# Performance work log

Hardware: AMD Instinct MI355X
Metric: run time of the kernel (lower is better)

## Reference

```python
import jax, jax.numpy as jnp
import numpy as np

D = 32  # embedding_dimension (TGN default memory_dimension == embedding_dimension)


def time_encode(t, w, b):
    # TGN TimeEncode: cos(t * w + b); t: [E] -> [E, D]
    return jnp.cos(t[:, None] * w[None, :] + b[None, :])


def setup_inputs() -> dict:
    key = jax.random.key(0)
    ks = jax.random.split(key, 24)
    N, B, E, F, NE = 1_000_000, 262_144, 1_048_576, 64, 500_000
    inp = {}
    # per-node-type memory tables (Mailbox memory)
    inp["mem_user"] = jax.random.normal(ks[0], (N, D), jnp.float32)
    inp["mem_item"] = jax.random.normal(ks[1], (N, D), jnp.float32)
    # active event node ids per type (memory lookup indices)
    inp["node_ids_user"] = jax.random.randint(ks[2], (B,), 0, N, jnp.int32)
    inp["node_ids_item"] = jax.random.randint(ks[3], (B,), 0, N, jnp.int32)
    # heterogeneous edge lists: user->item and item->user (indices into the B active nodes)
    inp["edge_src_ui"] = jax.random.randint(ks[4], (E,), 0, B, jnp.int32)
    inp["edge_dst_ui"] = jax.random.randint(ks[5], (E,), 0, B, jnp.int32)
    inp["edge_src_iu"] = jax.random.randint(ks[6], (E,), 0, B, jnp.int32)
    inp["edge_dst_iu"] = jax.random.randint(ks[7], (E,), 0, B, jnp.int32)
    inp["edge_idx_ui"] = jax.random.randint(ks[8], (E,), 0, NE, jnp.int32)
    inp["edge_idx_iu"] = jax.random.randint(ks[9], (E,), 0, NE, jnp.int32)
    inp["edge_rel_times_ui"] = jax.random.uniform(ks[10], (E,), jnp.float32) * 1000.0
    inp["edge_rel_times_iu"] = jax.random.uniform(ks[11], (E,), jnp.float32) * 1000.0
    inp["edge_feature"] = jax.random.normal(ks[12], (NE, F), jnp.float32)
    # per-node-type Linear(D, D, bias=False) == self.lin[node_type]
    s = 1.0 / np.sqrt(D)
    inp["W_user"] = jax.random.normal(ks[13], (D, D), jnp.float32) * s
    inp["W_item"] = jax.random.normal(ks[14], (D, D), jnp.float32) * s
    # per-edge-type Linear(F, D) == self.edge_feature_linear[edge_type]
    se = 1.0 / np.sqrt(F)
    inp["We_ui"] = jax.random.normal(ks[15], (F, D), jnp.float32) * se
    inp["be_ui"] = jnp.zeros((D,), jnp.float32)
    inp["We_iu"] = jax.random.normal(ks[16], (F, D), jnp.float32) * se
    inp["be_iu"] = jnp.zeros((D,), jnp.float32)
    # TimeEncode params (standard TGN init: 1/10^linspace)
    inp["time_w"] = jnp.asarray(1.0 / (10.0 ** np.linspace(0, 9, D)), jnp.float32)
    inp["time_b"] = jnp.zeros((D,), jnp.float32)
    # decoder(2*D -> 64 -> 16 -> 1), drop=0
    inp["dec_W1"] = jax.random.normal(ks[17], (2 * D, 64), jnp.float32) * (1.0 / np.sqrt(2 * D))
    inp["dec_b1"] = jnp.zeros((64,), jnp.float32)
    inp["dec_W2"] = jax.random.normal(ks[18], (64, 16), jnp.float32) * 0.125
    inp["dec_b2"] = jnp.zeros((16,), jnp.float32)
    inp["dec_W3"] = jax.random.normal(ks[19], (16, 1), jnp.float32) * 0.25
    inp["dec_b3"] = jnp.zeros((1,), jnp.float32)
    return inp


def reference(mem_user, mem_item, edge_feature, edge_rel_times_ui, edge_rel_times_iu,
              W_user, W_item, We_ui, be_ui, We_iu, be_iu, time_w, time_b,
              dec_W1, dec_b1, dec_W2, dec_b2, dec_W3, dec_b3,
              node_ids_user, node_ids_item, edge_src_ui, edge_dst_ui,
              edge_src_iu, edge_dst_iu, edge_idx_ui, edge_idx_iu):
    B = node_ids_user.shape[0]
    # memory lookup + per-node-type linear (self.lin[node_type], bias=False)
    h_user = mem_user[node_ids_user] @ W_user   # [B, D]
    h_item = mem_item[node_ids_item] @ W_item   # [B, D]
    # heterogeneous message passing: src memory + edge-feature linear + time encoding,
    # scattered (segment_sum) onto destination nodes per edge type
    msg_ui = (h_user[edge_src_ui]
              + edge_feature[edge_idx_ui] @ We_ui + be_ui
              + time_encode(edge_rel_times_ui, time_w, time_b))  # [E, D]
    agg_item = jax.ops.segment_sum(msg_ui, edge_dst_ui, num_segments=B)
    msg_iu = (h_item[edge_src_iu]
              + edge_feature[edge_idx_iu] @ We_iu + be_iu
              + time_encode(edge_rel_times_iu, time_w, time_b))  # [E, D]
    agg_user = jax.ops.segment_sum(msg_iu, edge_dst_iu, num_segments=B)
    hu = jax.nn.relu(h_user + agg_user)
    hi = jax.nn.relu(h_item + agg_item)
    # decoder `distance` on concatenated pair embeddings (2*D -> 64 -> 16 -> 1), drop=0
    z = jnp.concatenate([hu, hi], axis=-1)      # [B, 2D]
    x = jax.nn.relu(z @ dec_W1 + dec_b1)
    x = jax.nn.relu(x @ dec_W2 + dec_b2)
    return x @ dec_W3 + dec_b3                   # [B, 1]
```

## Files before the change

kernel.cpp:

```cpp
#include <hip/hip_runtime.h>

#define DEV __device__ __forceinline__

typedef __attribute__((ext_vector_type(8))) short short8;
typedef __attribute__((ext_vector_type(16))) float float16;
typedef __attribute__((ext_vector_type(4))) float f32x4;
typedef __attribute__((ext_vector_type(2))) unsigned int u32x2;
typedef __attribute__((ext_vector_type(4))) unsigned int u32x4;

DEV unsigned short f2bf(float x) {
    unsigned u = __float_as_uint(x);
    unsigned r = (u + 0x7FFFu + ((u >> 16) & 1u)) >> 16;
    return (unsigned short)r;
}
DEV unsigned pack_bf2(float a, float b) {
    return (unsigned)f2bf(a) | ((unsigned)f2bf(b) << 16);
}
DEV float bf2f(unsigned short v) {
    return __uint_as_float(((unsigned)v) << 16);
}
DEV float fastcos(float x) {
    float r = x * 0.15915494309189535f;
    r = r - floorf(r);
    return __builtin_amdgcn_cosf(r);
}

__global__ void prep_kernel(const float* __restrict__ W_user, const float* __restrict__ W_item,
                            const float* __restrict__ We_ui, const float* __restrict__ be_ui,
                            const float* __restrict__ We_iu, const float* __restrict__ be_iu,
                            const float* __restrict__ dW1, const float* __restrict__ dW2,
                            float* __restrict__ Wt_user, float* __restrict__ Wt_item,
                            unsigned short* __restrict__ Wb, float* __restrict__ bc,
                            float* __restrict__ W1t, float* __restrict__ W2t) {
    int t = threadIdx.x;
    for (int i = t; i < 1024; i += 256) {
        int k = i / 32, d = i % 32;
        Wt_user[d * 32 + k] = W_user[i];
        Wt_item[d * 32 + k] = W_item[i];
    }
    for (int i = t; i < 4096; i += 256) {
        int kt   = i >> 10;
        int rem  = i & 1023;
        int n2   = rem >> 9;
        int rem2 = rem & 511;
        int l    = rem2 >> 3;
        int ii   = rem2 & 7;
        int k = kt * 16 + (l >> 5) * 8 + ii;
        int n = (l & 31);
        float v = n2 ? We_iu[k * 32 + n] : We_ui[k * 32 + n];
        Wb[i] = f2bf(v);
    }
    for (int i = t; i < 64; i += 256)
        bc[i] = (i < 32) ? be_ui[i] : be_iu[i - 32];
    for (int i = t; i < 4096; i += 256) {
        int j = i / 64, k = i % 64;
        W1t[i] = dW1[k * 64 + j];
    }
    for (int i = t; i < 1024; i += 256) {
        int c = i / 64, j = i % 64;
        W2t[i] = dW2[j * 16 + c];
    }
}

__global__ __launch_bounds__(256) void node_linear_kernel(
        const float* __restrict__ mem, const int* __restrict__ ids,
        const float* __restrict__ Wt, float* __restrict__ h,
        unsigned short* __restrict__ h16, int B) {
    int r = blockIdx.x * 256 + threadIdx.x;
    if (r >= B) return;
    int id = ids[r];
    const f32x4* m4 = (const f32x4*)(mem + (size_t)id * 32);
    float m[32];
#pragma unroll
    for (int q = 0; q < 8; ++q) {
        f32x4 v = __builtin_nontemporal_load(m4 + q);
        m[4 * q + 0] = v[0]; m[4 * q + 1] = v[1]; m[4 * q + 2] = v[2]; m[4 * q + 3] = v[3];
    }
    float* hr = h + (size_t)r * 32;
    unsigned short* hr16 = h16 + (size_t)r * 32;
    for (int db = 0; db < 8; ++db) {
        float acc[4];
#pragma unroll
        for (int u = 0; u < 4; ++u) {
            const float* wr = Wt + (size_t)(db * 4 + u) * 32;
            float a = 0.f;
#pragma unroll
            for (int k = 0; k < 32; ++k) a = fmaf(m[k], wr[k], a);
            acc[u] = a;
        }
        f32x4 o; o[0] = acc[0]; o[1] = acc[1]; o[2] = acc[2]; o[3] = acc[3];
        __builtin_nontemporal_store(o, (f32x4*)(hr + db * 4));
        u32x2 p; p[0] = pack_bf2(acc[0], acc[1]); p[1] = pack_bf2(acc[2], acc[3]);
        *(u32x2*)(hr16 + db * 4) = p;
    }
}

__global__ __launch_bounds__(256) void proj_mfma_kernel(
        const float* __restrict__ feat, const unsigned short* __restrict__ Wb,
        const float* __restrict__ bc, unsigned short* __restrict__ proj, int NE) {
    __shared__ unsigned short lds[128 * 72];
    const int lane = threadIdx.x & 63;
    const int wave = threadIdx.x >> 6;
    const int col  = lane & 31;
    const int half = lane >> 5;

    short8 bfrag[8];
    const short8* wb8 = (const short8*)Wb;
#pragma unroll
    for (int f = 0; f < 8; ++f) bfrag[f] = wb8[f * 64 + lane];

    int r = blockIdx.x * 128 + wave * 32 + col;
    if (r >= NE) r = NE - 1;
    const float* fr = feat + (size_t)r * 64 + half * 8;
    short8 afrag[4];
#pragma unroll
    for (int t = 0; t < 4; ++t) {
        f32x4 a = __builtin_nontemporal_load((const f32x4*)(fr + t * 16));
        f32x4 b = __builtin_nontemporal_load((const f32x4*)(fr + t * 16 + 4));
        short8 s;
        s[0] = (short)f2bf(a[0]); s[1] = (short)f2bf(a[1]);
        s[2] = (short)f2bf(a[2]); s[3] = (short)f2bf(a[3]);
        s[4] = (short)f2bf(b[0]); s[5] = (short)f2bf(b[1]);
        s[6] = (short)f2bf(b[2]); s[7] = (short)f2bf(b[3]);
        afrag[t] = s;
    }

    float16 acc0, acc1;
    float b0 = bc[col], b1 = bc[32 + col];
#pragma unroll
    for (int i = 0; i < 16; ++i) { acc0[i] = b0; acc1[i] = b1; }
#pragma unroll
    for (int t = 0; t < 4; ++t) {
        acc0 = __builtin_amdgcn_mfma_f32_32x32x16_bf16(afrag[t], bfrag[t * 2 + 0], acc0, 0, 0, 0);
        acc1 = __builtin_amdgcn_mfma_f32_32x32x16_bf16(afrag[t], bfrag[t * 2 + 1], acc1, 0, 0, 0);
    }

#pragma unroll
    for (int reg = 0; reg < 16; ++reg) {
        int rl = wave * 32 + (reg & 3) + 8 * (reg >> 2) + 4 * half;
        lds[rl * 72 + col]      = f2bf(acc0[reg]);
        lds[rl * 72 + 32 + col] = f2bf(acc1[reg]);
    }
    __syncthreads();

    int trow = threadIdx.x >> 1, thalf = threadIdx.x & 1;
    int grow = blockIdx.x * 128 + trow;
    if (grow < NE) {
        const u32x4* lsrc = (const u32x4*)(lds + trow * 72 + thalf * 32);
        u32x4* gdst = (u32x4*)(proj + (size_t)grow * 64 + thalf * 32);
#pragma unroll
        for (int s = 0; s < 4; ++s) gdst[s] = lsrc[s];
    }
}

__global__ __launch_bounds__(256) void link_kernel(
        const int* __restrict__ src_ui, const int* __restrict__ dst_ui,
        const int* __restrict__ eidx_ui, const float* __restrict__ rt_ui,
        const int* __restrict__ src_iu, const int* __restrict__ dst_iu,
        const int* __restrict__ eidx_iu, const float* __restrict__ rt_iu,
        int* __restrict__ head, int4* __restrict__ edata, int E, int B) {
    int ge = blockIdx.x * 256 + threadIdx.x;
    if (ge >= 2 * E) return;
    int s, ix, d; float tv;
    if (ge < E) {
        s  = __builtin_nontemporal_load(src_ui + ge);
        ix = __builtin_nontemporal_load(eidx_ui + ge);
        tv = __builtin_nontemporal_load(rt_ui + ge);
        d  = __builtin_nontemporal_load(dst_ui + ge);
    } else {
        int e = ge - E;
        s  = __builtin_nontemporal_load(src_iu + e);
        ix = __builtin_nontemporal_load(eidx_iu + e);
        tv = __builtin_nontemporal_load(rt_iu + e);
        d  = __builtin_nontemporal_load(dst_iu + e) + B;
    }
    int nxt = atomicExch(head + d, ge);
    edata[ge] = make_int4(s, ix, __float_as_int(tv), nxt);
}

__global__ __launch_bounds__(256) void agg_kernel(
        const int4* __restrict__ edata, const int* __restrict__ head,
        const unsigned short* __restrict__ h16_user, const unsigned short* __restrict__ h16_item,
        const unsigned short* __restrict__ proj,
        float* __restrict__ agg_user, float* __restrict__ agg_item,
        const float* __restrict__ tw, const float* __restrict__ tb, int B) {
    int g = threadIdx.x >> 5, d = threadIdx.x & 31;
    int n = blockIdx.x * 8 + g;
    if (n >= 2 * B) return;
    int type = (n >= B);
    const unsigned short* h = type ? h16_item : h16_user;
    const unsigned short* pr = proj + (type ? 32 : 0) + d;
    float twd = tw[d], tbd = tb[d];
    float acc = 0.f;
    int e = head[n];
    while (e >= 0) {
        int4 cur = edata[e];
        float pv = bf2f(pr[(size_t)cur.y * 64]);
        float c  = fastcos(fmaf(__int_as_float(cur.z), twd, tbd));
        acc += bf2f(h[(size_t)cur.x * 32 + d]) + pv + c;
        e = cur.w;
    }
    if (type) agg_user[(size_t)(n - B) * 32 + d] = acc;
    else      agg_item[(size_t)n * 32 + d] = acc;
}

__global__ __launch_bounds__(256) void decoder_kernel(
        const float* __restrict__ h_user, const float* __restrict__ h_item,
        const float* __restrict__ agg_user, const float* __restrict__ agg_item,
        const float* __restrict__ W1t, const float* __restrict__ b1,
        const float* __restrict__ W2t, const float* __restrict__ b2,
        const float* __restrict__ W3, const float* __restrict__ b3,
        float* __restrict__ out, int B) {
    int i = blockIdx.x * 256 + threadIdx.x;
    if (i >= B) return;
    float z[64];
    {
        const f32x4* a4 = (const f32x4*)(h_user + (size_t)i * 32);
        const f32x4* b4 = (const f32x4*)(agg_user + (size_t)i * 32);
#pragma unroll
        for (int q = 0; q < 8; ++q) {
            f32x4 a = __builtin_nontemporal_load(a4 + q);
            f32x4 b = b4[q];
            z[4 * q + 0] = fmaxf(a[0] + b[0], 0.f);
            z[4 * q + 1] = fmaxf(a[1] + b[1], 0.f);
            z[4 * q + 2] = fmaxf(a[2] + b[2], 0.f);
            z[4 * q + 3] = fmaxf(a[3] + b[3], 0.f);
        }
    }
    {
        const f32x4* a4 = (const f32x4*)(h_item + (size_t)i * 32);
        const f32x4* b4 = (const f32x4*)(agg_item + (size_t)i * 32);
#pragma unroll
        for (int q = 0; q < 8; ++q) {
            f32x4 a = __builtin_nontemporal_load(a4 + q);
            f32x4 b = b4[q];
            z[32 + 4 * q + 0] = fmaxf(a[0] + b[0], 0.f);
            z[32 + 4 * q + 1] = fmaxf(a[1] + b[1], 0.f);
            z[32 + 4 * q + 2] = fmaxf(a[2] + b[2], 0.f);
            z[32 + 4 * q + 3] = fmaxf(a[3] + b[3], 0.f);
        }
    }
    float x2[16];
#pragma unroll
    for (int c = 0; c < 16; ++c) x2[c] = b2[c];
    for (int jb = 0; jb < 8; ++jb) {
        float a[8];
#pragma unroll
        for (int u = 0; u < 8; ++u) {
            int j = jb * 8 + u;
            const float* wr = W1t + (size_t)j * 64;
            float acc = b1[j];
#pragma unroll
            for (int k = 0; k < 64; ++k) acc = fmaf(z[k], wr[k], acc);
            a[u] = fmaxf(acc, 0.f);
        }
#pragma unroll
        for (int c = 0; c < 16; ++c) {
            const float* w2r = W2t + (size_t)c * 64 + jb * 8;
            float acc = x2[c];
#pragma unroll
            for (int u = 0; u < 8; ++u) acc = fmaf(a[u], w2r[u], acc);
            x2[c] = acc;
        }
    }
    float o = b3[0];
#pragma unroll
    for (int c = 0; c < 16; ++c) o = fmaf(fmaxf(x2[c], 0.f), W3[c], o);
    out[i] = o;
}

extern "C" void kernel_launch(void* const* d_in, const int* in_sizes, int n_in,
                              void* d_out, int out_size, void* d_ws, size_t ws_size,
                              hipStream_t stream) {
    const float* mem_user = (const float*)d_in[0];
    const float* mem_item = (const float*)d_in[1];
    const int*   ids_user = (const int*)d_in[2];
    const int*   ids_item = (const int*)d_in[3];
    const int*   src_ui   = (const int*)d_in[4];
    const int*   dst_ui   = (const int*)d_in[5];
    const int*   src_iu   = (const int*)d_in[6];
    const int*   dst_iu   = (const int*)d_in[7];
    const int*   eidx_ui  = (const int*)d_in[8];
    const int*   eidx_iu  = (const int*)d_in[9];
    const float* rt_ui    = (const float*)d_in[10];
    const float* rt_iu    = (const float*)d_in[11];
    const float* feat     = (const float*)d_in[12];
    const float* W_user   = (const float*)d_in[13];
    const float* W_item   = (const float*)d_in[14];
    const float* We_ui    = (const float*)d_in[15];
    const float* be_ui    = (const float*)d_in[16];
    const float* We_iu    = (const float*)d_in[17];
    const float* be_iu    = (const float*)d_in[18];
    const float* tw       = (const float*)d_in[19];
    const float* tb       = (const float*)d_in[20];
    const float* dW1      = (const float*)d_in[21];
    const float* db1      = (const float*)d_in[22];
    const float* dW2      = (const float*)d_in[23];
    const float* db2      = (const float*)d_in[24];
    const float* dW3      = (const float*)d_in[25];
    const float* db3      = (const float*)d_in[26];

    const int B  = in_sizes[2];
    const int E  = in_sizes[4];
    const int NE = in_sizes[12] / 64;
    const int NB2 = 2 * B;

    float* w = (float*)d_ws;
    const size_t hsz = (size_t)B * 32;
    float* h_user   = w;
    float* h_item   = h_user + hsz;
    float* agg_user = h_item + hsz;
    float* agg_item = agg_user + hsz;
    float* Wt_user  = agg_item + hsz;
    float* Wt_item  = Wt_user + 1024;
    unsigned short* Wb = (unsigned short*)(Wt_item + 1024);
    float* bc       = (float*)(Wb + 4096);
    float* W1t      = bc + 64;
    float* W2t      = W1t + 4096;
    unsigned short* proj = (unsigned short*)(W2t + 1024);
    int* head = (int*)(proj + (size_t)NE * 64);
    int4* edata = (int4*)(head + NB2);
    unsigned short* h16_user = (unsigned short*)(edata + (size_t)2 * E);
    unsigned short* h16_item = h16_user + hsz;

    prep_kernel<<<1, 256, 0, stream>>>(W_user, W_item, We_ui, be_ui, We_iu, be_iu, dW1, dW2,
                                       Wt_user, Wt_item, Wb, bc, W1t, W2t);
    (void)hipMemsetAsync(head, 0xFF, (size_t)NB2 * sizeof(int), stream);

    proj_mfma_kernel<<<(NE + 127) / 128, 256, 0, stream>>>(feat, Wb, bc, proj, NE);
    node_linear_kernel<<<(B + 255) / 256, 256, 0, stream>>>(mem_user, ids_user, Wt_user,
                                                            h_user, h16_user, B);
    node_linear_kernel<<<(B + 255) / 256, 256, 0, stream>>>(mem_item, ids_item, Wt_item,
                                                            h_item, h16_item, B);

    int e2blocks = (2 * E + 255) / 256;
    link_kernel<<<e2blocks, 256, 0, stream>>>(src_ui, dst_ui, eidx_ui, rt_ui,
                                              src_iu, dst_iu, eidx_iu, rt_iu,
                                              head, edata, E, B);
    agg_kernel<<<(NB2 + 7) / 8, 256, 0, stream>>>(edata, head, h16_user, h16_item, proj,
                                                  agg_user, agg_item, tw, tb, B);
    decoder_kernel<<<(B + 255) / 256, 256, 0, stream>>>(h_user, h_item, agg_user, agg_item,
                                                        W1t, db1, W2t, db2, dW3, db3,
                                                        (float*)d_out, B);
}
```

Baseline: 875.1 us.

## Split per-node edge linked lists into four chains for parallel traversal

The link kernel now spreads each destination node's edges over four separate list heads, chosen by the low bits of the edge id. The aggregation kernel then walks all four chains together, issuing up to four independent edata loads per iteration. This shortens each dependent pointer-chasing chain and raises memory-level parallelism, at the cost of a four-times-larger head array and memset, plus extra branching per iteration. Separately, nontemporal loads and stores in the node-linear and decoder kernels become ordinary accesses, so the h buffers can stay in cache for the decoder.

```diff
diff --git a/kernel.cpp b/kernel.cpp
--- a/kernel.cpp
+++ b/kernel.cpp
@@ -73,7 +73,7 @@
     float m[32];
 #pragma unroll
     for (int q = 0; q < 8; ++q) {
-        f32x4 v = __builtin_nontemporal_load(m4 + q);
+        f32x4 v = m4[q];
         m[4 * q + 0] = v[0]; m[4 * q + 1] = v[1]; m[4 * q + 2] = v[2]; m[4 * q + 3] = v[3];
     }
     float* hr = h + (size_t)r * 32;
@@ -89,7 +89,7 @@
             acc[u] = a;
         }
         f32x4 o; o[0] = acc[0]; o[1] = acc[1]; o[2] = acc[2]; o[3] = acc[3];
-        __builtin_nontemporal_store(o, (f32x4*)(hr + db * 4));
+        *(f32x4*)(hr + db * 4) = o;
         u32x2 p; p[0] = pack_bf2(acc[0], acc[1]); p[1] = pack_bf2(acc[2], acc[3]);
         *(u32x2*)(hr16 + db * 4) = p;
     }
@@ -174,12 +174,12 @@
         tv = __builtin_nontemporal_load(rt_iu + e);
         d  = __builtin_nontemporal_load(dst_iu + e) + B;
     }
-    int nxt = atomicExch(head + d, ge);
+    int nxt = atomicExch(head + (d << 2) + (ge & 3), ge);
     edata[ge] = make_int4(s, ix, __float_as_int(tv), nxt);
 }
 
 __global__ __launch_bounds__(256) void agg_kernel(
-        const int4* __restrict__ edata, const int* __restrict__ head,
+        const int4* __restrict__ edata, const int4* __restrict__ head4,
         const unsigned short* __restrict__ h16_user, const unsigned short* __restrict__ h16_item,
         const unsigned short* __restrict__ proj,
         float* __restrict__ agg_user, float* __restrict__ agg_item,
@@ -192,13 +192,34 @@
     const unsigned short* pr = proj + (type ? 32 : 0) + d;
     float twd = tw[d], tbd = tb[d];
     float acc = 0.f;
-    int e = head[n];
-    while (e >= 0) {
-        int4 cur = edata[e];
-        float pv = bf2f(pr[(size_t)cur.y * 64]);
-        float c  = fastcos(fmaf(__int_as_float(cur.z), twd, tbd));
-        acc += bf2f(h[(size_t)cur.x * 32 + d]) + pv + c;
-        e = cur.w;
+    int4 hd = head4[n];
+    int e0 = hd.x, e1 = hd.y, e2 = hd.z, e3 = hd.w;
+    while ((e0 & e1 & e2 & e3) >= 0) {
+        int4 c0, c1, c2, c3;
+        if (e0 >= 0) c0 = edata[e0];
+        if (e1 >= 0) c1 = edata[e1];
+        if (e2 >= 0) c2 = edata[e2];
+        if (e3 >= 0) c3 = edata[e3];
+        if (e0 >= 0) {
+            acc += bf2f(h[(size_t)c0.x * 32 + d]) + bf2f(pr[(size_t)c0.y * 64])
+                 + fastcos(fmaf(__int_as_float(c0.z), twd, tbd));
+            e0 = c0.w;
+        }
+        if (e1 >= 0) {
+            acc += bf2f(h[(size_t)c1.x * 32 + d]) + bf2f(pr[(size_t)c1.y * 64])
+                 + fastcos(fmaf(__int_as_float(c1.z), twd, tbd));
+            e1 = c1.w;
+        }
+        if (e2 >= 0) {
+            acc += bf2f(h[(size_t)c2.x * 32 + d]) + bf2f(pr[(size_t)c2.y * 64])
+                 + fastcos(fmaf(__int_as_float(c2.z), twd, tbd));
+            e2 = c2.w;
+        }
+        if (e3 >= 0) {
+            acc += bf2f(h[(size_t)c3.x * 32 + d]) + bf2f(pr[(size_t)c3.y * 64])
+                 + fastcos(fmaf(__int_as_float(c3.z), twd, tbd));
+            e3 = c3.w;
+        }
     }
     if (type) agg_user[(size_t)(n - B) * 32 + d] = acc;
     else      agg_item[(size_t)n * 32 + d] = acc;
@@ -219,8 +240,7 @@
         const f32x4* b4 = (const f32x4*)(agg_user + (size_t)i * 32);
 #pragma unroll
         for (int q = 0; q < 8; ++q) {
-            f32x4 a = __builtin_nontemporal_load(a4 + q);
-            f32x4 b = b4[q];
+            f32x4 a = a4[q], b = b4[q];
             z[4 * q + 0] = fmaxf(a[0] + b[0], 0.f);
             z[4 * q + 1] = fmaxf(a[1] + b[1], 0.f);
             z[4 * q + 2] = fmaxf(a[2] + b[2], 0.f);
@@ -232,8 +252,7 @@
         const f32x4* b4 = (const f32x4*)(agg_item + (size_t)i * 32);
 #pragma unroll
         for (int q = 0; q < 8; ++q) {
-            f32x4 a = __builtin_nontemporal_load(a4 + q);
-            f32x4 b = b4[q];
+            f32x4 a = a4[q], b = b4[q];
             z[32 + 4 * q + 0] = fmaxf(a[0] + b[0], 0.f);
             z[32 + 4 * q + 1] = fmaxf(a[1] + b[1], 0.f);
             z[32 + 4 * q + 2] = fmaxf(a[2] + b[2], 0.f);
@@ -319,13 +338,13 @@
     float* W2t      = W1t + 4096;
     unsigned short* proj = (unsigned short*)(W2t + 1024);
     int* head = (int*)(proj + (size_t)NE * 64);
-    int4* edata = (int4*)(head + NB2);
+    int4* edata = (int4*)(head + (size_t)NB2 * 4);
     unsigned short* h16_user = (unsigned short*)(edata + (size_t)2 * E);
     unsigned short* h16_item = h16_user + hsz;
 
     prep_kernel<<<1, 256, 0, stream>>>(W_user, W_item, We_ui, be_ui, We_iu, be_iu, dW1, dW2,
                                        Wt_user, Wt_item, Wb, bc, W1t, W2t);
-    (void)hipMemsetAsync(head, 0xFF, (size_t)NB2 * sizeof(int), stream);
+    (void)hipMemsetAsync(head, 0xFF, (size_t)NB2 * 4 * sizeof(int), stream);
 
     proj_mfma_kernel<<<(NE + 127) / 128, 256, 0, stream>>>(feat, Wb, bc, proj, NE);
     node_linear_kernel<<<(B + 255) / 256, 256, 0, stream>>>(mem_user, ids_user, Wt_user,
@@ -337,7 +356,8 @@
     link_kernel<<<e2blocks, 256, 0, stream>>>(src_ui, dst_ui, eidx_ui, rt_ui,
                                               src_iu, dst_iu, eidx_iu, rt_iu,
                                               head, edata, E, B);
-    agg_kernel<<<(NB2 + 7) / 8, 256, 0, stream>>>(edata, head, h16_user, h16_item, proj,
+    agg_kernel<<<(NB2 + 7) / 8, 256, 0, stream>>>(edata, (const int4*)head,
+                                                  h16_user, h16_item, proj,
                                                   agg_user, agg_item, tw, tb, B);
     decoder_kernel<<<(B + 255) / 256, 256, 0, stream>>>(h_user, h_item, agg_user, agg_item,
                                                         W1t, db1, W2t, db2, dW3, db3,
```

Result: no change. 862.5 us (-1.4%).

## Replace linked-list edge chains with counting-sort CSR for aggregation

Applied to the files above, without the earlier changes.

Replaces the atomicExch linked-list construction with a histogram, a three-pass prefix scan, and an atomic scatter that builds a per-destination permutation (CSR-like). The aggregation kernel then iterates over contiguous index ranges, unrolled by four, so independent gathers can be in flight at once instead of chasing a serial pointer chain. Several nontemporal loads and stores are also changed to regular accesses. It adds extra kernel launches, a second pass over the destination arrays, and one more indirection per edge (perm then edata).

```diff
diff --git a/kernel.cpp b/kernel.cpp
--- a/kernel.cpp
+++ b/kernel.cpp
@@ -73,7 +73,7 @@
     float m[32];
 #pragma unroll
     for (int q = 0; q < 8; ++q) {
-        f32x4 v = __builtin_nontemporal_load(m4 + q);
+        f32x4 v = m4[q];
         m[4 * q + 0] = v[0]; m[4 * q + 1] = v[1]; m[4 * q + 2] = v[2]; m[4 * q + 3] = v[3];
     }
     float* hr = h + (size_t)r * 32;
@@ -89,7 +89,7 @@
             acc[u] = a;
         }
         f32x4 o; o[0] = acc[0]; o[1] = acc[1]; o[2] = acc[2]; o[3] = acc[3];
-        __builtin_nontemporal_store(o, (f32x4*)(hr + db * 4));
+        *(f32x4*)(hr + db * 4) = o;
         u32x2 p; p[0] = pack_bf2(acc[0], acc[1]); p[1] = pack_bf2(acc[2], acc[3]);
         *(u32x2*)(hr16 + db * 4) = p;
     }
@@ -153,12 +153,12 @@
     }
 }
 
-__global__ __launch_bounds__(256) void link_kernel(
+__global__ __launch_bounds__(256) void hist_pack_kernel(
         const int* __restrict__ src_ui, const int* __restrict__ dst_ui,
         const int* __restrict__ eidx_ui, const float* __restrict__ rt_ui,
         const int* __restrict__ src_iu, const int* __restrict__ dst_iu,
         const int* __restrict__ eidx_iu, const float* __restrict__ rt_iu,
-        int* __restrict__ head, int4* __restrict__ edata, int E, int B) {
+        int* __restrict__ cnt, int4* __restrict__ edata, int E, int B) {
     int ge = blockIdx.x * 256 + threadIdx.x;
     if (ge >= 2 * E) return;
     int s, ix, d; float tv;
@@ -166,20 +166,87 @@
         s  = __builtin_nontemporal_load(src_ui + ge);
         ix = __builtin_nontemporal_load(eidx_ui + ge);
         tv = __builtin_nontemporal_load(rt_ui + ge);
-        d  = __builtin_nontemporal_load(dst_ui + ge);
+        d  = dst_ui[ge];
     } else {
         int e = ge - E;
         s  = __builtin_nontemporal_load(src_iu + e);
         ix = __builtin_nontemporal_load(eidx_iu + e);
         tv = __builtin_nontemporal_load(rt_iu + e);
-        d  = __builtin_nontemporal_load(dst_iu + e) + B;
-    }
-    int nxt = atomicExch(head + d, ge);
-    edata[ge] = make_int4(s, ix, __float_as_int(tv), nxt);
+        d  = dst_iu[e] + B;
+    }
+    atomicAdd(cnt + d, 1);
+    edata[ge] = make_int4(s, ix, __float_as_int(tv), 0);
+}
+
+__global__ __launch_bounds__(256) void scan1_kernel(
+        const int* __restrict__ cnt, int* __restrict__ base,
+        int* __restrict__ part, int n) {
+    __shared__ int sh[256];
+    int t = threadIdx.x;
+    int i0 = blockIdx.x * 1024 + t * 4;
+    int c0 = (i0 + 0 < n) ? cnt[i0 + 0] : 0;
+    int c1 = (i0 + 1 < n) ? cnt[i0 + 1] : 0;
+    int c2 = (i0 + 2 < n) ? cnt[i0 + 2] : 0;
+    int c3 = (i0 + 3 < n) ? cnt[i0 + 3] : 0;
+    int s = c0 + c1 + c2 + c3;
+    sh[t] = s; __syncthreads();
+    for (int off = 1; off < 256; off <<= 1) {
+        int v = sh[t];
+        int a = (t >= off) ? sh[t - off] : 0;
+        __syncthreads();
+        sh[t] = v + a;
+        __syncthreads();
+    }
+    int excl = sh[t] - s;
+    if (t == 255) part[blockIdx.x] = sh[255];
+    if (i0 + 0 < n) base[i0 + 0] = excl; excl += c0;
+    if (i0 + 1 < n) base[i0 + 1] = excl; excl += c1;
+    if (i0 + 2 < n) base[i0 + 2] = excl; excl += c2;
+    if (i0 + 3 < n) base[i0 + 3] = excl;
+}
+
+__global__ __launch_bounds__(256) void scan2_kernel(int* __restrict__ part, int n) {
+    __shared__ int sh[256];
+    int t = threadIdx.x;
+    int i0 = t * 16;
+    int c[16];
+#pragma unroll
+    for (int q = 0; q < 16; ++q) c[q] = (i0 + q < n) ? part[i0 + q] : 0;
+    int s = 0;
+#pragma unroll
+    for (int q = 0; q < 16; ++q) s += c[q];
+    sh[t] = s; __syncthreads();
+    for (int off = 1; off < 256; off <<= 1) {
+        int v = sh[t];
+        int a = (t >= off) ? sh[t - off] : 0;
+        __syncthreads();
+        sh[t] = v + a;
+        __syncthreads();
+    }
+    int excl = sh[t] - s;
+#pragma unroll
+    for (int q = 0; q < 16; ++q) { if (i0 + q < n) part[i0 + q] = excl; excl += c[q]; }
+}
+
+__global__ __launch_bounds__(256) void scan3_kernel(
+        int* __restrict__ base, const int* __restrict__ part, int n) {
+    int i = blockIdx.x * 256 + threadIdx.x;
+    if (i < n) base[i] += part[i >> 10];
+}
+
+__global__ __launch_bounds__(256) void scatter_perm_kernel(
+        const int* __restrict__ dst_ui, const int* __restrict__ dst_iu,
+        int* __restrict__ base, int* __restrict__ perm, int E, int B) {
+    int ge = blockIdx.x * 256 + threadIdx.x;
+    if (ge >= 2 * E) return;
+    int d = (ge < E) ? dst_ui[ge] : (dst_iu[ge - E] + B);
+    int pos = atomicAdd(base + d, 1);
+    perm[pos] = ge;
 }
 
 __global__ __launch_bounds__(256) void agg_kernel(
-        const int4* __restrict__ edata, const int* __restrict__ head,
+        const int4* __restrict__ edata, const int* __restrict__ base,
+        const int* __restrict__ perm,
         const unsigned short* __restrict__ h16_user, const unsigned short* __restrict__ h16_item,
         const unsigned short* __restrict__ proj,
         float* __restrict__ agg_user, float* __restrict__ agg_item,
@@ -192,13 +259,31 @@
     const unsigned short* pr = proj + (type ? 32 : 0) + d;
     float twd = tw[d], tbd = tb[d];
     float acc = 0.f;
-    int e = head[n];
-    while (e >= 0) {
-        int4 cur = edata[e];
-        float pv = bf2f(pr[(size_t)cur.y * 64]);
-        float c  = fastcos(fmaf(__int_as_float(cur.z), twd, tbd));
-        acc += bf2f(h[(size_t)cur.x * 32 + d]) + pv + c;
-        e = cur.w;
+    int b1 = base[n];
+    int b0 = n ? base[n - 1] : 0;
+    int j = b0;
+    for (; j + 4 <= b1; j += 4) {
+        int p0 = perm[j], p1 = perm[j + 1], p2 = perm[j + 2], p3 = perm[j + 3];
+        int4 c0 = edata[p0], c1 = edata[p1], c2 = edata[p2], c3 = edata[p3];
+        float h0 = bf2f(h[(size_t)c0.x * 32 + d]);
+        float h1 = bf2f(h[(size_t)c1.x * 32 + d]);
+        float h2 = bf2f(h[(size_t)c2.x * 32 + d]);
+        float h3 = bf2f(h[(size_t)c3.x * 32 + d]);
+        float v0 = bf2f(pr[(size_t)c0.y * 64]);
+        float v1 = bf2f(pr[(size_t)c1.y * 64]);
+        float v2 = bf2f(pr[(size_t)c2.y * 64]);
+        float v3 = bf2f(pr[(size_t)c3.y * 64]);
+        float t0 = fastcos(fmaf(__int_as_float(c0.z), twd, tbd));
+        float t1 = fastcos(fmaf(__int_as_float(c1.z), twd, tbd));
+        float t2 = fastcos(fmaf(__int_as_float(c2.z), twd, tbd));
+        float t3 = fastcos(fmaf(__int_as_float(c3.z), twd, tbd));
+        acc += (h0 + v0 + t0) + (h1 + v1 + t1) + (h2 + v2 + t2) + (h3 + v3 + t3);
+    }
+    for (; j < b1; ++j) {
+        int p = perm[j];
+        int4 c = edata[p];
+        acc += bf2f(h[(size_t)c.x * 32 + d]) + bf2f(pr[(size_t)c.y * 64])
+             + fastcos(fmaf(__int_as_float(c.z), twd, tbd));
     }
     if (type) agg_user[(size_t)(n - B) * 32 + d] = acc;
     else      agg_item[(size_t)n * 32 + d] = acc;
@@ -219,8 +304,7 @@
         const f32x4* b4 = (const f32x4*)(agg_user + (size_t)i * 32);
 #pragma unroll
         for (int q = 0; q < 8; ++q) {
-            f32x4 a = __builtin_nontemporal_load(a4 + q);
-            f32x4 b = b4[q];
+            f32x4 a = a4[q], b = b4[q];
             z[4 * q + 0] = fmaxf(a[0] + b[0], 0.f);
             z[4 * q + 1] = fmaxf(a[1] + b[1], 0.f);
             z[4 * q + 2] = fmaxf(a[2] + b[2], 0.f);
@@ -232,8 +316,7 @@
         const f32x4* b4 = (const f32x4*)(agg_item + (size_t)i * 32);
 #pragma unroll
         for (int q = 0; q < 8; ++q) {
-            f32x4 a = __builtin_nontemporal_load(a4 + q);
-            f32x4 b = b4[q];
+            f32x4 a = a4[q], b = b4[q];
             z[32 + 4 * q + 0] = fmaxf(a[0] + b[0], 0.f);
             z[32 + 4 * q + 1] = fmaxf(a[1] + b[1], 0.f);
             z[32 + 4 * q + 2] = fmaxf(a[2] + b[2], 0.f);
@@ -318,14 +401,17 @@
     float* W1t      = bc + 64;
     float* W2t      = W1t + 4096;
     unsigned short* proj = (unsigned short*)(W2t + 1024);
-    int* head = (int*)(proj + (size_t)NE * 64);
-    int4* edata = (int4*)(head + NB2);
+    int* cnt  = (int*)(proj + (size_t)NE * 64);
+    int* base = cnt + NB2;
+    int* part = base + NB2;
+    int* perm = part + 4096;
+    int4* edata = (int4*)(perm + (size_t)2 * E);
     unsigned short* h16_user = (unsigned short*)(edata + (size_t)2 * E);
     unsigned short* h16_item = h16_user + hsz;
 
     prep_kernel<<<1, 256, 0, stream>>>(W_user, W_item, We_ui, be_ui, We_iu, be_iu, dW1, dW2,
                                        Wt_user, Wt_item, Wb, bc, W1t, W2t);
-    (void)hipMemsetAsync(head, 0xFF, (size_t)NB2 * sizeof(int), stream);
+    (void)hipMemsetAsync(cnt, 0, (size_t)NB2 * sizeof(int), stream);
 
     proj_mfma_kernel<<<(NE + 127) / 128, 256, 0, stream>>>(feat, Wb, bc, proj, NE);
     node_linear_kernel<<<(B + 255) / 256, 256, 0, stream>>>(mem_user, ids_user, Wt_user,
@@ -334,10 +420,16 @@
                                                             h_item, h16_item, B);
 
     int e2blocks = (2 * E + 255) / 256;
-    link_kernel<<<e2blocks, 256, 0, stream>>>(src_ui, dst_ui, eidx_ui, rt_ui,
-                                              src_iu, dst_iu, eidx_iu, rt_iu,
-                                              head, edata, E, B);
-    agg_kernel<<<(NB2 + 7) / 8, 256, 0, stream>>>(edata, head, h16_user, h16_item, proj,
+    hist_pack_kernel<<<e2blocks, 256, 0, stream>>>(src_ui, dst_ui, eidx_ui, rt_ui,
+                                                   src_iu, dst_iu, eidx_iu, rt_iu,
+                                                   cnt, edata, E, B);
+    int nblk1 = (NB2 + 1023) / 1024;
+    scan1_kernel<<<nblk1, 256, 0, stream>>>(cnt, base, part, NB2);
+    scan2_kernel<<<1, 256, 0, stream>>>(part, nblk1);
+    scan3_kernel<<<(NB2 + 255) / 256, 256, 0, stream>>>(base, part, NB2);
+    scatter_perm_kernel<<<e2blocks, 256, 0, stream>>>(dst_ui, dst_iu, base, perm, E, B);
+    agg_kernel<<<(NB2 + 7) / 8, 256, 0, stream>>>(edata, base, perm,
+                                                  h16_user, h16_item, proj,
                                                   agg_user, agg_item, tw, tb, B);
     decoder_kernel<<<(B + 255) / 256, 256, 0, stream>>>(h_user, h_item, agg_user, agg_item,
                                                         W1t, db1, W2t, db2, dW3, db3,
```

After: 998.2 us. 14.1% more time.
